# Performance work log

Measured on AMD Instinct MI355X. Metric: run time of the kernel, lower is better.

## Reference

```python
import jax, jax.numpy as jnp
import numpy as np

B, N, D, NH, HID = 64, 197, 768, 8, 3072
LN_EPS = 1e-5

def _ln(x, g, b):
    m = x.mean(-1, keepdims=True)
    v = x.var(-1, keepdims=True)
    return (x - m) / jnp.sqrt(v + LN_EPS) * g + b

def _so8_gate(x, w, bias, scale, eps):
    # x: [B,N,Dg]; eps: [B,N,8 heads,4 planes]. Closed-form SO(8) planar rotations
    # (equivalent to matrix_exp of the 4 sparse 2x2-block generators, composed).
    Bb, Nn, Dg = x.shape
    hd = Dg // 8
    xp = x @ w.T + bias                      # orth_monitor Linear
    xh = xp.reshape(Bb, Nn, 8, hd)           # [B,N,H,hd]
    x8 = xh[..., :8]                         # first 8 channels per head
    ang = eps * scale                        # angles = randn * rotation_scale
    c, s = jnp.cos(ang), jnp.sin(ang)        # [B,N,8,4]
    ev, od = x8[..., 0::2], x8[..., 1::2]    # plane components
    rot8 = jnp.stack([ev * c - od * s, ev * s + od * c], -1).reshape(Bb, Nn, 8, 8)
    rotated = jnp.concatenate([rot8, xh[..., 8:]], -1)
    err = jnp.linalg.norm(rot8 - x8, axis=-1).mean(-1)  # fro norm per head, mean over heads -> [B,N]
    return rotated.reshape(Bb, Nn, Dg) + x, err

def _adapter(x, w, bias, scale, ln_g, ln_b, eps):
    y, err = _so8_gate(x, w, bias, scale, eps)
    return _ln(y, ln_g, ln_b) + x, err

def setup_inputs():
    key = jax.random.key(0)
    ks = jax.random.split(key, 26)
    rn = lambda k, shp, s=0.02: (jax.random.normal(k, shp) * s).astype(jnp.float32)
    z = lambda shp: jnp.zeros(shp, jnp.float32)
    o = lambda shp: jnp.ones(shp, jnp.float32)
    return {
        'x': jax.random.normal(ks[0], (B, N, D), jnp.float32),
        'qkv_w': rn(ks[1], (3 * D, D)), 'qkv_b': z((3 * D,)),
        'proj_w': rn(ks[2], (D, D)), 'proj_b': z((D,)),
        'norm1_g': o((D,)), 'norm1_b': z((D,)),
        'norm2_g': o((D,)), 'norm2_b': z((D,)),
        'orth_w_a': rn(ks[3], (D, D)), 'orth_b_a': z((D,)),
        'scale_a': o((1,)), 'ln_g_a': o((D,)), 'ln_b_a': z((D,)),
        'orth_w_m': rn(ks[4], (HID, HID)), 'orth_b_m': z((HID,)),
        'scale_m': o((1,)), 'ln_g_m': o((HID,)), 'ln_b_m': z((HID,)),
        'fc1_w': rn(ks[5], (HID, D)), 'fc1_b': z((HID,)),
        'fc2_w': rn(ks[6], (D, HID)), 'fc2_b': z((D,)),
        'eps_a': jax.random.normal(ks[7], (B, N, 8, 4), jnp.float32),
        'eps_m': jax.random.normal(ks[8], (B, N, 8, 4), jnp.float32),
    }

def reference(x, qkv_w, qkv_b, proj_w, proj_b, norm1_g, norm1_b, norm2_g, norm2_b,
              orth_w_a, orth_b_a, scale_a, ln_g_a, ln_b_a,
              orth_w_m, orth_b_m, scale_m, ln_g_m, ln_b_m,
              fc1_w, fc1_b, fc2_w, fc2_b, eps_a, eps_m):
    hd = D // NH
    # attention branch
    x1 = _ln(x, norm1_g, norm1_b)
    qkv = (x1 @ qkv_w.T + qkv_b).reshape(B, N, 3, NH, hd).transpose(2, 0, 3, 1, 4)
    q, k, v = qkv[0], qkv[1], qkv[2]
    attn = jax.nn.softmax(jnp.einsum('bhqd,bhkd->bhqk', q, k) * hd ** -0.5, -1)
    ctx = jnp.einsum('bhqk,bhkd->bhqd', attn, v).transpose(0, 2, 1, 3).reshape(B, N, D)
    ctx = ctx @ proj_w.T + proj_b
    xa, e1 = _adapter(ctx, orth_w_a, orth_b_a, scale_a, ln_g_a, ln_b_a, eps_a)
    x = x + xa
    # mlp branch with SO(8) adapter on hidden
    x2 = _ln(x, norm2_g, norm2_b)
    h = jax.nn.gelu(x2 @ fc1_w.T + fc1_b, approximate=False)
    h, e2 = _adapter(h, orth_w_m, orth_b_m, scale_m, ln_g_m, ln_b_m, eps_m)
    xm = h @ fc2_w.T + fc2_b
    x = x + xm
    return x, e1 + e2
```

## Files before the change

### kernel.cpp

```cpp
#include <hip/hip_runtime.h>
#include <hip/hip_bf16.h>
#include <math.h>

#define MROWS (64*197)
#define DMODEL 768
#define DHID   3072

typedef __hip_bfloat16 bf16;
using bf16x8 = __attribute__((ext_vector_type(8))) short;
using f32x4  = __attribute__((ext_vector_type(4))) float;

__device__ __forceinline__ float b2f(bf16 v) { return __bfloat162float(v); }
__device__ __forceinline__ short f2bs(float f) {
    bf16 h = __float2bfloat16(f);
    return *reinterpret_cast<short*>(&h);
}
__device__ __forceinline__ void b8f(bf16x8 v, float* f) {
#pragma unroll
    for (int j = 0; j < 8; ++j)
        f[j] = __uint_as_float(((unsigned int)(unsigned short)v[j]) << 16);
}
__device__ __forceinline__ bf16x8 f8b(const float* f) {
    bf16x8 r;
#pragma unroll
    for (int j = 0; j < 8; ++j) r[j] = f2bs(f[j]);
    return r;
}
__device__ __forceinline__ float gelu_exact(float v) {
    return 0.5f * v * (1.0f + erff(v * 0.70710678118654752f));
}
__device__ __forceinline__ void st1(bf16* p, float v) { *p = __float2bfloat16(v); }
__device__ __forceinline__ void st1(float* p, float v) { *p = v; }

__device__ __forceinline__ void gl_lds16(const short* g, short* l) {
    __builtin_amdgcn_global_load_lds(
        (const __attribute__((address_space(1))) void*)g,
        (__attribute__((address_space(3))) void*)l, 16, 0, 0);
}

__global__ __launch_bounds__(256) void cvt_all_kernel(
        const float* __restrict__ s0, const float* __restrict__ s1,
        const float* __restrict__ s2, const float* __restrict__ s3,
        const float* __restrict__ s4, const float* __restrict__ s5,
        short* __restrict__ dst) {
    const int b0 = 442368, b1 = 589824, b2 = 737280,
              b3 = 3096576, b4 = 3686400, b5 = 4276224;
    int i = blockIdx.x * 256 + threadIdx.x;
    if (i >= b5) return;
    const float* src; int off;
    if      (i < b0) { src = s0; off = i; }
    else if (i < b1) { src = s1; off = i - b0; }
    else if (i < b2) { src = s2; off = i - b1; }
    else if (i < b3) { src = s3; off = i - b2; }
    else if (i < b4) { src = s4; off = i - b3; }
    else             { src = s5; off = i - b4; }
    float4 v = ((const float4*)src)[off];
    ((short4*)dst)[i] = make_short4(f2bs(v.x), f2bs(v.y), f2bs(v.z), f2bs(v.w));
}

__global__ __launch_bounds__(256) void ln1_kernel(const float* __restrict__ in,
        const float* __restrict__ g, const float* __restrict__ b,
        bf16* __restrict__ out, int Dg) {
    int row = blockIdx.x;
    int n4 = Dg >> 2;
    const float4* xr = (const float4*)(in + (size_t)row * Dg);
    float s = 0.f, s2 = 0.f;
    for (int c = threadIdx.x; c < n4; c += 256) {
        float4 v = xr[c];
        s += v.x + v.y + v.z + v.w;
        s2 += v.x * v.x + v.y * v.y + v.z * v.z + v.w * v.w;
    }
    __shared__ float r1[4], r2[4];
    for (int off = 32; off; off >>= 1) { s += __shfl_down(s, off, 64); s2 += __shfl_down(s2, off, 64); }
    if ((threadIdx.x & 63) == 0) { r1[threadIdx.x >> 6] = s; r2[threadIdx.x >> 6] = s2; }
    __syncthreads();
    s  = r1[0] + r1[1] + r1[2] + r1[3];
    s2 = r2[0] + r2[1] + r2[2] + r2[3];
    float mean = s / Dg;
    float rstd = rsqrtf(s2 / Dg - mean * mean + 1e-5f);
    short4* yr = (short4*)(out + (size_t)row * Dg);
    const float4* g4 = (const float4*)g;
    const float4* b4 = (const float4*)b;
    for (int c = threadIdx.x; c < n4; c += 256) {
        float4 v = xr[c], gg = g4[c], bb = b4[c];
        yr[c] = make_short4(f2bs((v.x - mean) * rstd * gg.x + bb.x),
                            f2bs((v.y - mean) * rstd * gg.y + bb.y),
                            f2bs((v.z - mean) * rstd * gg.z + bb.z),
                            f2bs((v.w - mean) * rstd * gg.w + bb.w));
    }
}


#define G256_BAR        __builtin_amdgcn_s_barrier()
#define G256_LGKM0      asm volatile("s_waitcnt lgkmcnt(0)" ::: "memory")
#define G256_VM4        asm volatile("s_waitcnt vmcnt(4)" ::: "memory")
#define G256_VM0        asm volatile("s_waitcnt vmcnt(0)" ::: "memory")

#define G256_STAGE_A(BUF, SET, KT) do {                                        \
    _Pragma("unroll")                                                          \
    for (int qq = 0; qq < 2; ++qq) {                                           \
        int rl = qq * 128 + (SET) * 64 + (tid >> 3);                           \
        int rg = m0 + rl; if (rg > Mr - 1) rg = Mr - 1;                        \
        int jc = (tid & 7) ^ (rl & 7);                                         \
        gl_lds16(A + (size_t)rg * Kc + (KT) + jc * 8,                          \
                 As[BUF] + rl * 64 + (tid & 7) * 8);                           \
    } } while (0)

#define G256_STAGE_B(BUF, SET, KT) do {                                        \
    _Pragma("unroll")                                                          \
    for (int qq = 0; qq < 2; ++qq) {                                           \
        int rl = (qq * 2 + (tid >> 8)) * 64 + (SET) * 32 + ((tid & 255) >> 3); \
        int jc = (tid & 7) ^ (rl & 7);                                         \
        gl_lds16(W + (size_t)(n0 + rl) * Kc + (KT) + jc * 8,                   \
                 Bs[BUF] + rl * 64 + (tid & 7) * 8);                           \
    } } while (0)

#define G256_LDA(BUF, MQ) do {                                                 \
    _Pragma("unroll")                                                          \
    for (int i = 0; i < 4; ++i) {                                              \
        int row = wm * 128 + (MQ) * 64 + i * 16 + l16;                         \
        const short* rp = As[BUF] + row * 64;                                  \
        _Pragma("unroll")                                                      \
        for (int ks = 0; ks < 2; ++ks)                                         \
            a[i][ks] = *(const bf16x8*)(rp + (((ks * 4 + quad) ^ (row & 7)) << 3)); \
    } } while (0)

#define G256_LDB(BUF, NQ) do {                                                 \
    _Pragma("unroll")                                                          \
    for (int j = 0; j < 2; ++j) {                                              \
        int row = wn * 64 + (NQ) * 32 + j * 16 + l16;                          \
        const short* rp = Bs[BUF] + row * 64;                                  \
        _Pragma("unroll")                                                      \
        for (int ks = 0; ks < 2; ++ks)                                         \
            b[j][ks] = *(const bf16x8*)(rp + (((ks * 4 + quad) ^ (row & 7)) << 3)); \
    } } while (0)

#define G256_MMA(MQ, NQ) do {                                                  \
    __builtin_amdgcn_s_setprio(1);                                             \
    _Pragma("unroll")                                                          \
    for (int i = 0; i < 4; ++i)                                                \
        _Pragma("unroll")                                                      \
        for (int j = 0; j < 2; ++j)                                            \
            _Pragma("unroll")                                                  \
            for (int ks = 0; ks < 2; ++ks)                                     \
                acc[(MQ) * 4 + i][(NQ) * 2 + j] =                              \
                    __builtin_amdgcn_mfma_f32_16x16x32_bf16(                   \
                        a[i][ks], b[j][ks], acc[(MQ) * 4 + i][(NQ) * 2 + j], 0, 0, 0); \
    __builtin_amdgcn_s_setprio(0);                                             \
} while (0)

template<int MODE, typename TC>
__global__ __launch_bounds__(512, 2) void gemm256(const short* __restrict__ A,
        const short* __restrict__ W, const float* __restrict__ bias,
        const bf16* __restrict__ resid, TC* __restrict__ C,
        int Mr, int Nc, int Kc, int ntn)
{
    __shared__ short As[2][256 * 64];
    __shared__ short Bs[2][256 * 64];
    const int tid  = threadIdx.x;
    const int lane = tid & 63, wave = tid >> 6;
    const int wm = wave >> 2, wn = wave & 3;
    const int quad = lane >> 4, l16 = lane & 15;

    const int nwg = gridDim.x;
    const int qd = nwg >> 3, rm = nwg & 7;
    const int xcd = blockIdx.x & 7, lin = blockIdx.x >> 3;
    const int wg = (xcd < rm ? xcd * (qd + 1) : rm * (qd + 1) + (xcd - rm) * qd) + lin;
    const int m0 = (wg / ntn) * 256, n0 = (wg % ntn) * 256;

    f32x4 acc[8][4];
#pragma unroll
    for (int i = 0; i < 8; ++i)
#pragma unroll
        for (int j = 0; j < 4; ++j) acc[i][j] = (f32x4){0.f, 0.f, 0.f, 0.f};
    bf16x8 a[4][2], b[2][2];

    const int niter = Kc >> 7;

    G256_STAGE_A(0, 0, 0);  G256_STAGE_B(0, 1, 0);
    G256_STAGE_A(0, 1, 0);  G256_STAGE_B(0, 0, 0);
    G256_STAGE_A(1, 0, 64); G256_STAGE_B(1, 1, 64);
    G256_VM4;
    G256_BAR;

    for (int it = 0; it < niter; ++it) {
        const int kT = it * 128;
        const bool pre = (it + 1 < niter);
        G256_LDA(0, 0); G256_LDB(0, 0);
        G256_STAGE_A(1, 1, kT + 64);
        G256_BAR; G256_LGKM0;
        G256_MMA(0, 0);
        G256_LDB(0, 1);
        G256_STAGE_B(1, 0, kT + 64);
        G256_BAR; G256_LGKM0;
        G256_MMA(0, 1);
        G256_LDA(0, 1);
        if (pre) G256_STAGE_A(0, 0, kT + 128);
        G256_BAR; G256_LGKM0;
        G256_MMA(1, 1);
        G256_LDB(0, 0);
        if (pre) G256_STAGE_B(0, 1, kT + 128);
        if (pre) { G256_VM4; } else { G256_VM0; }
        G256_BAR; G256_LGKM0;
        G256_MMA(1, 0);
        G256_LDA(1, 0); G256_LDB(1, 0);
        if (pre) G256_STAGE_A(0, 1, kT + 128);
        G256_BAR; G256_LGKM0;
        G256_MMA(0, 0);
        G256_LDB(1, 1);
        if (pre) G256_STAGE_B(0, 0, kT + 128);
        G256_BAR; G256_LGKM0;
        G256_MMA(0, 1);
        G256_LDA(1, 1);
        if (pre) G256_STAGE_A(1, 0, kT + 192);
        G256_BAR; G256_LGKM0;
        G256_MMA(1, 1);
        G256_LDB(1, 0);
        if (pre) G256_STAGE_B(1, 1, kT + 192);
        if (pre) { G256_VM4; } else { G256_VM0; }
        G256_BAR; G256_LGKM0;
        G256_MMA(1, 0);
    }

#pragma unroll
    for (int fm = 0; fm < 8; ++fm)
#pragma unroll
        for (int r = 0; r < 4; ++r) {
            int row = m0 + wm * 128 + fm * 16 + quad * 4 + r;
            if (row >= Mr) continue;
#pragma unroll
            for (int fn = 0; fn < 4; ++fn) {
                int col = n0 + wn * 64 + fn * 16 + l16;
                float v = acc[fm][fn][r] + bias[col];
                if (MODE == 1) v = gelu_exact(v);
                if (MODE == 2) v += b2f(resid[(size_t)row * Nc + col]);
                st1(C + (size_t)row * Nc + col, v);
            }
        }
}

template<int MODE, typename TC>
__global__ __launch_bounds__(256) void gemm_bf(const short* __restrict__ A,
        const short* __restrict__ W, const float* __restrict__ bias,
        const bf16* __restrict__ resid, TC* __restrict__ C,
        int Mr, int Nc, int Kc)
{
    __shared__ short Abuf[128 * 64];
    __shared__ short Bbuf[128 * 64];
    const int tid  = threadIdx.x;
    const int lane = tid & 63, wave = tid >> 6;
    const int wm = wave & 1, wn = wave >> 1;
    const int quad = lane >> 4, l16 = lane & 15;
    const int m0 = blockIdx.y * 128, n0 = blockIdx.x * 128;

    f32x4 acc[4][4];
#pragma unroll
    for (int i = 0; i < 4; ++i)
#pragma unroll
        for (int j = 0; j < 4; ++j) acc[i][j] = (f32x4){0.f, 0.f, 0.f, 0.f};

    for (int k0 = 0; k0 < Kc; k0 += 64) {
        __syncthreads();
#pragma unroll
        for (int q = 0; q < 4; ++q) {
            int c = q * 256 + tid;
            int row = c >> 3;
            int j = (c & 7) ^ (row & 7);
            int rowA = m0 + row;
            if (rowA > Mr - 1) rowA = Mr - 1;
            gl_lds16(A + (size_t)rowA * Kc + k0 + j * 8, Abuf + c * 8);
        }
#pragma unroll
        for (int q = 0; q < 4; ++q) {
            int c = q * 256 + tid;
            int row = c >> 3;
            int j = (c & 7) ^ (row & 7);
            gl_lds16(W + (size_t)(n0 + row) * Kc + k0 + j * 8, Bbuf + c * 8);
        }
        __syncthreads();
#pragma unroll
        for (int t = 0; t < 2; ++t) {
            bf16x8 fa[4], fb[4];
#pragma unroll
            for (int i = 0; i < 4; ++i) {
                int r = wm * 64 + i * 16 + l16;
                fa[i] = *(const bf16x8*)(Abuf + r * 64 + (((t * 4 + quad) ^ (r & 7)) << 3));
            }
#pragma unroll
            for (int j = 0; j < 4; ++j) {
                int r = wn * 64 + j * 16 + l16;
                fb[j] = *(const bf16x8*)(Bbuf + r * 64 + (((t * 4 + quad) ^ (r & 7)) << 3));
            }
#pragma unroll
            for (int i = 0; i < 4; ++i)
#pragma unroll
                for (int j = 0; j < 4; ++j)
                    acc[i][j] = __builtin_amdgcn_mfma_f32_16x16x32_bf16(fa[i], fb[j], acc[i][j], 0, 0, 0);
        }
    }

#pragma unroll
    for (int i = 0; i < 4; ++i)
#pragma unroll
        for (int r = 0; r < 4; ++r) {
            int row = m0 + wm * 64 + i * 16 + quad * 4 + r;
            if (row >= Mr) continue;
#pragma unroll
            for (int j = 0; j < 4; ++j) {
                int col = n0 + wn * 64 + j * 16 + l16;
                float v = acc[i][j][r] + bias[col];
                if (MODE == 1) v = gelu_exact(v);
                if (MODE == 2) v += b2f(resid[(size_t)row * Nc + col]);
                st1(C + (size_t)row * Nc + col, v);
            }
        }
}

template<int MODE, typename TC>
__global__ __launch_bounds__(256) void gemm_f32b(const short* __restrict__ A,
        const float* __restrict__ W, const float* __restrict__ bias,
        const bf16* __restrict__ resid, TC* __restrict__ C,
        int Mr, int Nc, int Kc)
{
    __shared__ short Abuf[128 * 32];
    __shared__ short Bbuf[128 * 32];
    const int tid  = threadIdx.x;
    const int lane = tid & 63, wave = tid >> 6;
    const int wm = wave & 1, wn = wave >> 1;
    const int quad = lane >> 4, l16 = lane & 15;
    const int m0 = blockIdx.y * 128, n0 = blockIdx.x * 128;
    f32x4 acc[4][4];
#pragma unroll
    for (int i = 0; i < 4; ++i)
#pragma unroll
        for (int j = 0; j < 4; ++j) acc[i][j] = (f32x4){0.f, 0.f, 0.f, 0.f};
    const int brow = tid >> 3;
    const int bk   = (tid & 7) * 4;
    for (int k0 = 0; k0 < Kc; k0 += 32) {
        float4 wv[4];
#pragma unroll
        for (int s = 0; s < 4; ++s)
            wv[s] = *(const float4*)(W + (size_t)(n0 + s * 32 + brow) * Kc + k0 + bk);
        __syncthreads();
#pragma unroll
        for (int q = 0; q < 2; ++q) {
            int c = q * 256 + tid;
            int rowA = m0 + (c >> 2);
            if (rowA > Mr - 1) rowA = Mr - 1;
            gl_lds16(A + (size_t)rowA * Kc + k0 + (c & 3) * 8, Abuf + c * 8);
        }
#pragma unroll
        for (int s = 0; s < 4; ++s) {
            short4 h = make_short4(f2bs(wv[s].x), f2bs(wv[s].y), f2bs(wv[s].z), f2bs(wv[s].w));
            *(short4*)(Bbuf + (s * 32 + brow) * 32 + bk) = h;
        }
        __syncthreads();
        bf16x8 fa[4], fb[4];
#pragma unroll
        for (int i = 0; i < 4; ++i)
            fa[i] = *(const bf16x8*)(Abuf + (wm * 64 + i * 16 + l16) * 32 + quad * 8);
#pragma unroll
        for (int j = 0; j < 4; ++j)
            fb[j] = *(const bf16x8*)(Bbuf + (wn * 64 + j * 16 + l16) * 32 + quad * 8);
#pragma unroll
        for (int i = 0; i < 4; ++i)
#pragma unroll
            for (int j = 0; j < 4; ++j)
                acc[i][j] = __builtin_amdgcn_mfma_f32_16x16x32_bf16(fa[i], fb[j], acc[i][j], 0, 0, 0);
    }
#pragma unroll
    for (int i = 0; i < 4; ++i)
#pragma unroll
        for (int r = 0; r < 4; ++r) {
            int row = m0 + wm * 64 + i * 16 + quad * 4 + r;
            if (row >= Mr) continue;
#pragma unroll
            for (int j = 0; j < 4; ++j) {
                int col = n0 + wn * 64 + j * 16 + l16;
                float v = acc[i][j][r] + bias[col];
                if (MODE == 1) v = gelu_exact(v);
                if (MODE == 2) v += b2f(resid[(size_t)row * Nc + col]);
                st1(C + (size_t)row * Nc + col, v);
            }
        }
}

__global__ __launch_bounds__(256) void attn_mfma(const bf16* __restrict__ qkv,
        bf16* __restrict__ ctx) {
    const int NS = 197;
    const int KST = 104;
    const int VST = 232;
    __shared__ short Kbuf[224 * KST];
    __shared__ short Vt[96 * VST];
    __shared__ short Pbuf[4][16 * VST];
    const int b = blockIdx.x >> 3, h = blockIdx.x & 7;
    const short* base = (const short*)qkv + (size_t)b * NS * 2304 + h * 96;
    const int tid = threadIdx.x;

    for (int c = tid; c < NS * 12; c += 256) {
        int key = c / 12, dc = c % 12;
        bf16x8 v = *(const bf16x8*)(base + (size_t)key * 2304 + 768 + dc * 8);
        *(bf16x8*)(Kbuf + key * KST + dc * 8) = v;
    }
    for (int c = tid; c < 27 * 12; c += 256) {
        int key = NS + c / 12, dc = c % 12;
        *(bf16x8*)(Kbuf + key * KST + dc * 8) = (bf16x8){0, 0, 0, 0, 0, 0, 0, 0};
    }
    for (int c = tid; c < NS * 12; c += 256) {
        int key = c / 12, dc = c % 12;
        bf16x8 v = *(const bf16x8*)(base + (size_t)key * 2304 + 1536 + dc * 8);
#pragma unroll
        for (int j = 0; j < 8; ++j) Vt[(dc * 8 + j) * VST + key] = v[j];
    }
    for (int c = tid; c < 96 * 27; c += 256) {
        int d = c / 27, key = NS + c % 27;
        Vt[d * VST + key] = 0;
    }
    __syncthreads();

    const int wave = tid >> 6, lane = tid & 63;
    const int quad = lane >> 4, l16 = lane & 15;
    short* P = &Pbuf[wave][0];

    for (int qt = wave; qt < 13; qt += 4) {
        int qrow = qt * 16 + l16; if (qrow > NS - 1) qrow = NS - 1;
        bf16x8 fq[3];
#pragma unroll
        for (int kc = 0; kc < 3; ++kc)
            fq[kc] = *(const bf16x8*)(base + (size_t)qrow * 2304 + kc * 32 + quad * 8);
        f32x4 s[14];
#pragma unroll
        for (int nt = 0; nt < 14; ++nt) {
            s[nt] = (f32x4){0.f, 0.f, 0.f, 0.f};
#pragma unroll
            for (int kc = 0; kc < 3; ++kc) {
                bf16x8 fk = *(const bf16x8*)(Kbuf + (nt * 16 + l16) * KST + kc * 32 + quad * 8);
                s[nt] = __builtin_amdgcn_mfma_f32_16x16x32_bf16(fq[kc], fk, s[nt], 0, 0, 0);
            }
        }
        const float sc = 0.10206207261596577f;
        float mx[4] = {-1e30f, -1e30f, -1e30f, -1e30f};
#pragma unroll
        for (int nt = 0; nt < 14; ++nt) {
            bool valid = nt * 16 + l16 < NS;
#pragma unroll
            for (int r = 0; r < 4; ++r) {
                float v = s[nt][r] * sc;
                s[nt][r] = v;
                if (valid) mx[r] = fmaxf(mx[r], v);
            }
        }
#pragma unroll
        for (int m = 1; m < 16; m <<= 1)
#pragma unroll
            for (int r = 0; r < 4; ++r) mx[r] = fmaxf(mx[r], __shfl_xor(mx[r], m, 64));
        float l[4] = {0.f, 0.f, 0.f, 0.f};
#pragma unroll
        for (int nt = 0; nt < 14; ++nt) {
            bool valid = nt * 16 + l16 < NS;
#pragma unroll
            for (int r = 0; r < 4; ++r) {
                float e = valid ? __expf(s[nt][r] - mx[r]) : 0.f;
                l[r] += e;
                P[(quad * 4 + r) * VST + nt * 16 + l16] = f2bs(e);
            }
        }
#pragma unroll
        for (int m = 1; m < 16; m <<= 1)
#pragma unroll
            for (int r = 0; r < 4; ++r) l[r] += __shfl_xor(l[r], m, 64);
        __asm__ volatile("s_waitcnt lgkmcnt(0)" ::: "memory");
        f32x4 o[6];
#pragma unroll
        for (int nt = 0; nt < 6; ++nt) o[nt] = (f32x4){0.f, 0.f, 0.f, 0.f};
#pragma unroll
        for (int kc = 0; kc < 7; ++kc) {
            bf16x8 fp = *(const bf16x8*)(P + l16 * VST + kc * 32 + quad * 8);
#pragma unroll
            for (int nt = 0; nt < 6; ++nt) {
                bf16x8 fv = *(const bf16x8*)(Vt + (nt * 16 + l16) * VST + kc * 32 + quad * 8);
                o[nt] = __builtin_amdgcn_mfma_f32_16x16x32_bf16(fp, fv, o[nt], 0, 0, 0);
            }
        }
        float inv[4];
#pragma unroll
        for (int r = 0; r < 4; ++r) inv[r] = 1.f / l[r];
#pragma unroll
        for (int r = 0; r < 4; ++r) {
            int q = qt * 16 + quad * 4 + r;
            if (q >= NS) continue;
            bf16* orow = ctx + ((size_t)(b * NS + q)) * 768 + h * 96;
#pragma unroll
            for (int nt = 0; nt < 6; ++nt)
                orow[nt * 16 + l16] = __float2bfloat16(o[nt][r] * inv[r]);
        }
    }
}

template<bool OUTER, bool FINAL, bool FLN2>
__global__ __launch_bounds__(256) void adapter_finish(
        const bf16* __restrict__ xp, const bf16* __restrict__ xin,
        const float* __restrict__ xouter, const float* __restrict__ eps,
        const float* __restrict__ scale_p, const float* __restrict__ g,
        const float* __restrict__ bta, bf16* __restrict__ out,
        float* __restrict__ e_acc, float* __restrict__ e_out,
        const float* __restrict__ g2, const float* __restrict__ b2,
        bf16* __restrict__ out2, int Dg)
{
    extern __shared__ float smem[];
    float* y = smem;
    float* diff2 = smem + Dg;
    float* red = diff2 + 64;
    float* r1 = red + 8;
    float* r2 = red + 12;
    int row = blockIdx.x;
    int hd = Dg >> 3;
    int hd8 = hd >> 3;
    int n8 = Dg >> 3;
    const bf16* xpr = xp + (size_t)row * Dg;
    const bf16* xir = xin + (size_t)row * Dg;
    int tid = threadIdx.x;
    if (tid < 64) {
        int hh = tid >> 3, i = tid & 7, p = i >> 1;
        float ang = eps[((size_t)row * 8 + hh) * 4 + p] * scale_p[0];
        float c = cosf(ang), sn = sinf(ang);
        int base = hh * hd;
        float ev = b2f(xpr[base + 2 * p]), od = b2f(xpr[base + 2 * p + 1]);
        float r = (i & 1) ? (ev * sn + od * c) : (ev * c - od * sn);
        float d = r - b2f(xpr[base + i]);
        diff2[tid] = d * d;
        y[base + i] = r + b2f(xir[base + i]);
    }
    for (int c8 = tid; c8 < n8; c8 += 256) {
        if (c8 % hd8 == 0) continue;
        float a[8], bvx[8];
        b8f(*(const bf16x8*)(xpr + c8 * 8), a);
        b8f(*(const bf16x8*)(xir + c8 * 8), bvx);
#pragma unroll
        for (int j = 0; j < 8; ++j) y[c8 * 8 + j] = a[j] + bvx[j];
    }
    __syncthreads();
    if (tid < 8) {
        float t = 0.f;
#pragma unroll
        for (int i = 0; i < 8; ++i) t += diff2[tid * 8 + i];
        red[tid] = sqrtf(t);
    }
    float s = 0.f, s2 = 0.f;
    for (int c = tid; c < Dg; c += 256) { float v = y[c]; s += v; s2 += v * v; }
    for (int off = 32; off; off >>= 1) { s += __shfl_down(s, off, 64); s2 += __shfl_down(s2, off, 64); }
    if ((tid & 63) == 0) { r1[tid >> 6] = s; r2[tid >> 6] = s2; }
    __syncthreads();
    s  = r1[0] + r1[1] + r1[2] + r1[3];
    s2 = r2[0] + r2[1] + r2[2] + r2[3];
    float mean = s / Dg;
    float rstd = rsqrtf(s2 / Dg - mean * mean + 1e-5f);
    if (tid == 0) {
        float e = (red[0] + red[1] + red[2] + red[3] + red[4] + red[5] + red[6] + red[7]) * 0.125f;
        if (FINAL) e_out[row] = e_acc[row] + e;
        else       e_acc[row] = e;
    }
    bf16* outr = out + (size_t)row * Dg;
    const float4* g4 = (const float4*)g;
    const float4* bt4 = (const float4*)bta;
    const float4* xo4 = OUTER ? (const float4*)(xouter + (size_t)row * Dg) : nullptr;
    float sB = 0.f, sB2 = 0.f;
    for (int c8 = tid; c8 < n8; c8 += 256) {
        float xi[8];
        b8f(*(const bf16x8*)(xir + c8 * 8), xi);
        float4 gg0 = g4[c8 * 2], gg1 = g4[c8 * 2 + 1];
        float4 bb0 = bt4[c8 * 2], bb1 = bt4[c8 * 2 + 1];
        float gv[8] = {gg0.x, gg0.y, gg0.z, gg0.w, gg1.x, gg1.y, gg1.z, gg1.w};
        float bv[8] = {bb0.x, bb0.y, bb0.z, bb0.w, bb1.x, bb1.y, bb1.z, bb1.w};
        float vv[8];
#pragma unroll
        for (int j = 0; j < 8; ++j)
            vv[j] = (y[c8 * 8 + j] - mean) * rstd * gv[j] + bv[j] + xi[j];
        if (OUTER) {
            float4 o0 = xo4[c8 * 2], o1 = xo4[c8 * 2 + 1];
            float ov[8] = {o0.x, o0.y, o0.z, o0.w, o1.x, o1.y, o1.z, o1.w};
#pragma unroll
            for (int j = 0; j < 8; ++j) vv[j] += ov[j];
        }
        *(bf16x8*)(outr + c8 * 8) = f8b(vv);
        if (FLN2) {
#pragma unroll
            for (int j = 0; j < 8; ++j) {
                y[c8 * 8 + j] = vv[j];
                sB += vv[j]; sB2 += vv[j] * vv[j];
            }
        }
    }
    if (FLN2) {
        __syncthreads();
        for (int off = 32; off; off >>= 1) { sB += __shfl_down(sB, off, 64); sB2 += __shfl_down(sB2, off, 64); }
        if ((tid & 63) == 0) { r1[tid >> 6] = sB; r2[tid >> 6] = sB2; }
        __syncthreads();
        sB  = r1[0] + r1[1] + r1[2] + r1[3];
        sB2 = r2[0] + r2[1] + r2[2] + r2[3];
        float mean2 = sB / Dg;
        float rstd2 = rsqrtf(sB2 / Dg - mean2 * mean2 + 1e-5f);
        bf16* o2r = out2 + (size_t)row * Dg;
        const float4* g24 = (const float4*)g2;
        const float4* b24 = (const float4*)b2;
        for (int c8 = tid; c8 < n8; c8 += 256) {
            float4 gg0 = g24[c8 * 2], gg1 = g24[c8 * 2 + 1];
            float4 bb0 = b24[c8 * 2], bb1 = b24[c8 * 2 + 1];
            float gv[8] = {gg0.x, gg0.y, gg0.z, gg0.w, gg1.x, gg1.y, gg1.z, gg1.w};
            float bv[8] = {bb0.x, bb0.y, bb0.z, bb0.w, bb1.x, bb1.y, bb1.z, bb1.w};
            float vv[8];
#pragma unroll
            for (int j = 0; j < 8; ++j)
                vv[j] = (y[c8 * 8 + j] - mean2) * rstd2 * gv[j] + bv[j];
            *(bf16x8*)(o2r + c8 * 8) = f8b(vv);
        }
    }
}

extern "C" void kernel_launch(void* const* d_in, const int* in_sizes, int n_in,
                              void* d_out, int out_size, void* d_ws, size_t ws_size,
                              hipStream_t stream) {
    (void)in_sizes; (void)n_in; (void)out_size;
    const int M = MROWS;
    const size_t S_D = (size_t)M * DMODEL;
    const size_t S_H = (size_t)M * DHID;

    const float* x      = (const float*)d_in[0];
    const float* qkv_w  = (const float*)d_in[1];
    const float* qkv_b  = (const float*)d_in[2];
    const float* proj_w = (const float*)d_in[3];
    const float* proj_b = (const float*)d_in[4];
    const float* n1g    = (const float*)d_in[5];
    const float* n1b    = (const float*)d_in[6];
    const float* n2g    = (const float*)d_in[7];
    const float* n2b    = (const float*)d_in[8];
    const float* wa     = (const float*)d_in[9];
    const float* ba     = (const float*)d_in[10];
    const float* sca    = (const float*)d_in[11];
    const float* lga    = (const float*)d_in[12];
    const float* lba    = (const float*)d_in[13];
    const float* wm     = (const float*)d_in[14];
    const float* bm     = (const float*)d_in[15];
    const float* scm    = (const float*)d_in[16];
    const float* lgm    = (const float*)d_in[17];
    const float* lbm    = (const float*)d_in[18];
    const float* f1w    = (const float*)d_in[19];
    const float* f1b    = (const float*)d_in[20];
    const float* f2w    = (const float*)d_in[21];
    const float* f2b    = (const float*)d_in[22];
    const float* eps_a  = (const float*)d_in[23];
    const float* eps_m  = (const float*)d_in[24];

    float* out_x = (float*)d_out;
    float* out_e = out_x + S_D;

    bf16* R1 = (bf16*)d_ws;
    bf16* R2 = R1 + S_H;
    bf16* R3 = R2 + S_H;
    float* E = (float*)(R3 + S_D);

    const size_t n_qkv = (size_t)2304 * 768, n_proj = (size_t)768 * 768,
                 n_wa = (size_t)768 * 768, n_wm = (size_t)3072 * 3072,
                 n_f1 = (size_t)3072 * 768, n_f2 = (size_t)768 * 3072;
    const size_t base_bytes = (2 * S_H + S_D) * 2 + (size_t)M * 4;
    const size_t w_elems = n_qkv + n_proj + n_wa + n_wm + n_f1 + n_f2;
    const bool cache_w = ws_size >= base_bytes + w_elems * 2;

    short* WB    = (short*)((char*)d_ws + base_bytes);
    short* wb_qkv = WB;
    short* wb_proj = wb_qkv + n_qkv;
    short* wb_wa  = wb_proj + n_proj;
    short* wb_wm  = wb_wa + n_wa;
    short* wb_f1  = wb_wm + n_wm;
    short* wb_f2  = wb_f1 + n_f1;

    const int GY = (M + 127) / 128;
    const int GY256 = (M + 255) / 256;
    const size_t lds_a = (DMODEL + 96) * sizeof(float);
    const size_t lds_m = (DHID + 96) * sizeof(float);

    if (cache_w) {
        cvt_all_kernel<<<(4276224 + 255) / 256, 256, 0, stream>>>(
            qkv_w, proj_w, wa, wm, f1w, f2w, WB);
        ln1_kernel<<<M, 256, 0, stream>>>(x, n1g, n1b, R1, DMODEL);
        gemm_bf<0, bf16><<<dim3(2304 / 128, GY), 256, 0, stream>>>(
            (const short*)R1, wb_qkv, qkv_b, nullptr, R2, M, 2304, DMODEL);
        attn_mfma<<<64 * 8, 256, 0, stream>>>(R2, R1);
        gemm_bf<0, bf16><<<dim3(DMODEL / 128, GY), 256, 0, stream>>>(
            (const short*)R1, wb_proj, proj_b, nullptr, R2, M, DMODEL, DMODEL);
        gemm_bf<0, bf16><<<dim3(DMODEL / 128, GY), 256, 0, stream>>>(
            (const short*)R2, wb_wa, ba, nullptr, R1, M, DMODEL, DMODEL);
        adapter_finish<true, false, true><<<M, 256, lds_a, stream>>>(
            R1, R2, x, eps_a, sca, lga, lba, R3, E, nullptr, n2g, n2b, R2, DMODEL);
        gemm_bf<1, bf16><<<dim3(DHID / 128, GY), 256, 0, stream>>>(
            (const short*)R2, wb_f1, f1b, nullptr, R1, M, DHID, DMODEL);
        gemm256<0, bf16><<<dim3((DHID / 256) * GY256), 512, 0, stream>>>(
            (const short*)R1, wb_wm, bm, nullptr, R2, M, DHID, DHID, DHID / 256);
        adapter_finish<false, true, false><<<M, 256, lds_m, stream>>>(
            R2, R1, nullptr, eps_m, scm, lgm, lbm, R1, E, out_e, nullptr, nullptr, nullptr, DHID);
        gemm_bf<2, float><<<dim3(DMODEL / 128, GY), 256, 0, stream>>>(
            (const short*)R1, wb_f2, f2b, R3, out_x, M, DMODEL, DHID);
    } else {
        ln1_kernel<<<M, 256, 0, stream>>>(x, n1g, n1b, R1, DMODEL);
        gemm_f32b<0, bf16><<<dim3(2304 / 128, GY), 256, 0, stream>>>(
            (const short*)R1, qkv_w, qkv_b, nullptr, R2, M, 2304, DMODEL);
        attn_mfma<<<64 * 8, 256, 0, stream>>>(R2, R1);
        gemm_f32b<0, bf16><<<dim3(DMODEL / 128, GY), 256, 0, stream>>>(
            (const short*)R1, proj_w, proj_b, nullptr, R2, M, DMODEL, DMODEL);
        gemm_f32b<0, bf16><<<dim3(DMODEL / 128, GY), 256, 0, stream>>>(
            (const short*)R2, wa, ba, nullptr, R1, M, DMODEL, DMODEL);
        adapter_finish<true, false, true><<<M, 256, lds_a, stream>>>(
            R1, R2, x, eps_a, sca, lga, lba, R3, E, nullptr, n2g, n2b, R2, DMODEL);
        gemm_f32b<1, bf16><<<dim3(DHID / 128, GY), 256, 0, stream>>>(
            (const short*)R2, f1w, f1b, nullptr, R1, M, DHID, DMODEL);
        gemm_f32b<0, bf16><<<dim3(DHID / 128, GY), 256, 0, stream>>>(
            (const short*)R1, wm, bm, nullptr, R2, M, DHID, DHID);
        adapter_finish<false, true, false><<<M, 256, lds_m, stream>>>(
            R2, R1, nullptr, eps_m, scm, lgm, lbm, R1, E, out_e, nullptr, nullptr, nullptr, DHID);
        gemm_f32b<2, float><<<dim3(DMODEL / 128, GY), 256, 0, stream>>>(
            (const short*)R1, f2w, f2b, R3, out_x, M, DMODEL, DHID);
    }
}
```

Measured before the change: 899.2 us.

## Restructure GEMM main loop to halve barriers and pin schedule with sched_barrier

Rewrites the 256x256 GEMM's software pipeline so each pair of A/B global-to-LDS stages is issued together and a workgroup barrier happens only every two MMA sub-steps instead of every one. Adds sched_barrier(0) fences so the compiler cannot reorder LDS reads, MMAs and waits across phase boundaries. The goal is to cut barrier stalls in the K-loop. The trade-off is that larger batches of outstanding loads and the new vmcnt placement may expose more latency or create LDS hazards if the buffer reuse ordering is wrong.

```diff
diff --git a/kernel.cpp b/kernel.cpp
--- a/kernel.cpp
+++ b/kernel.cpp
@@ -92,6 +92,7 @@
 
 
 #define G256_BAR        __builtin_amdgcn_s_barrier()
+#define G256_SB0        __builtin_amdgcn_sched_barrier(0)
 #define G256_LGKM0      asm volatile("s_waitcnt lgkmcnt(0)" ::: "memory")
 #define G256_VM4        asm volatile("s_waitcnt vmcnt(4)" ::: "memory")
 #define G256_VM0        asm volatile("s_waitcnt vmcnt(0)" ::: "memory")
@@ -177,49 +178,50 @@
 
     const int niter = Kc >> 7;
 
-    G256_STAGE_A(0, 0, 0);  G256_STAGE_B(0, 1, 0);
-    G256_STAGE_A(0, 1, 0);  G256_STAGE_B(0, 0, 0);
+    G256_STAGE_A(0, 0, 0);  G256_STAGE_B(0, 0, 0);
+    G256_STAGE_A(0, 1, 0);  G256_STAGE_B(0, 1, 0);
     G256_STAGE_A(1, 0, 64); G256_STAGE_B(1, 1, 64);
     G256_VM4;
-    G256_BAR;
 
     for (int it = 0; it < niter; ++it) {
         const int kT = it * 128;
         const bool pre = (it + 1 < niter);
+        G256_BAR; G256_SB0;
         G256_LDA(0, 0); G256_LDB(0, 0);
-        G256_STAGE_A(1, 1, kT + 64);
-        G256_BAR; G256_LGKM0;
+        G256_STAGE_A(1, 1, kT + 64); G256_STAGE_B(1, 0, kT + 64);
+        G256_LGKM0; G256_SB0;
         G256_MMA(0, 0);
         G256_LDB(0, 1);
-        G256_STAGE_B(1, 0, kT + 64);
-        G256_BAR; G256_LGKM0;
+        G256_LGKM0; G256_SB0;
         G256_MMA(0, 1);
+        if (pre) { G256_VM4; } else { G256_VM0; }
+        G256_BAR; G256_SB0;
         G256_LDA(0, 1);
-        if (pre) G256_STAGE_A(0, 0, kT + 128);
-        G256_BAR; G256_LGKM0;
+        if (pre) { G256_STAGE_A(0, 0, kT + 128); G256_STAGE_B(0, 1, kT + 128); }
+        G256_LGKM0; G256_SB0;
         G256_MMA(1, 1);
         G256_LDB(0, 0);
-        if (pre) G256_STAGE_B(0, 1, kT + 128);
+        G256_LGKM0; G256_SB0;
+        G256_MMA(1, 0);
         if (pre) { G256_VM4; } else { G256_VM0; }
-        G256_BAR; G256_LGKM0;
-        G256_MMA(1, 0);
+        G256_BAR; G256_SB0;
         G256_LDA(1, 0); G256_LDB(1, 0);
-        if (pre) G256_STAGE_A(0, 1, kT + 128);
-        G256_BAR; G256_LGKM0;
+        if (pre) { G256_STAGE_A(0, 1, kT + 128); G256_STAGE_B(0, 0, kT + 128); }
+        G256_LGKM0; G256_SB0;
         G256_MMA(0, 0);
         G256_LDB(1, 1);
-        if (pre) G256_STAGE_B(0, 0, kT + 128);
-        G256_BAR; G256_LGKM0;
+        G256_LGKM0; G256_SB0;
         G256_MMA(0, 1);
+        if (pre) { G256_VM4; } else { G256_VM0; }
+        G256_BAR; G256_SB0;
         G256_LDA(1, 1);
-        if (pre) G256_STAGE_A(1, 0, kT + 192);
-        G256_BAR; G256_LGKM0;
+        if (pre) { G256_STAGE_A(1, 0, kT + 192); G256_STAGE_B(1, 1, kT + 192); }
+        G256_LGKM0; G256_SB0;
         G256_MMA(1, 1);
         G256_LDB(1, 0);
-        if (pre) G256_STAGE_B(1, 1, kT + 192);
+        G256_LGKM0; G256_SB0;
+        G256_MMA(1, 0);
         if (pre) { G256_VM4; } else { G256_VM0; }
-        G256_BAR; G256_LGKM0;
-        G256_MMA(1, 0);
     }
 
 #pragma unroll
```

New measurement: 914.2 us. About the same (+1.7%).
